# Kernel optimization log

Hardware: AMD Instinct MI355X
Metric: run time of the kernel (lower is better)

Reference implementation:

```python
import jax, jax.numpy as jnp
import numpy as np

B, H, W = 2, 512, 512
HID, NHKD, HEADS, KD, CD = 64, 128, 8, 16, 64
MAX_SHAPE = 512

def _conv(x, w, b=None, pad=0, groups=1):
    y = jax.lax.conv_general_dilated(x, w, (1, 1), [(pad, pad), (pad, pad)],
                                     dimension_numbers=('NCHW', 'OIHW', 'NCHW'),
                                     feature_group_count=groups)
    return y if b is None else y + b[None, :, None, None]

def _gelu(x):
    return jax.nn.gelu(x, approximate=False)  # torch nn.GELU default is exact erf

def _bn(x, s, t):
    # inference-mode BatchNorm folded to per-channel scale/shift
    return x * s[None, :, None, None] + t[None, :, None, None]

def _dyn_pos(xm, pe):
    # xm: (B, C, N); pe: (1, C, MAX_SHAPE); linear interp (align_corners=False) when N != MAX_SHAPE
    N = xm.shape[-1]
    if N != pe.shape[-1]:
        pe = jax.image.resize(pe, (1, pe.shape[1], N), method='linear')
    return xm + pe

def _sdpa(q, k, v):
    # q, k, v: (B, heads, L=key_dim, E=H); scale = 1/sqrt(E) as in F.scaled_dot_product_attention
    scale = 1.0 / np.sqrt(q.shape[-1])
    attn = jax.nn.softmax(jnp.einsum('bhie,bhje->bhij', q, k) * scale, axis=-1)
    return jnp.einsum('bhij,bhje->bhie', attn, v)

def setup_inputs():
    key = jax.random.key(0)
    ks = jax.random.split(key, 26)
    rn = lambda i, shp, sc=1.0: jax.random.normal(ks[i], shp, jnp.float32) * sc
    return {
        'x': rn(0, (B, HID, H, W)),
        'shortcut': rn(1, (B, CD, H, W)),
        'ln_w': jnp.ones((CD,), jnp.float32),
        'ln_b': jnp.zeros((CD,), jnp.float32),
        'dproj_dw_w': rn(2, (CD, 1, 3, 3), 0.2),
        'dproj_bn_s': 1.0 + rn(3, (CD,), 0.1),
        'dproj_bn_t': rn(4, (CD,), 0.1),
        'dproj_pw_w': rn(5, (2 * HID, CD, 1, 1), 0.125),
        'dproj_pw_b': rn(6, (2 * HID,), 0.05),
        'q_dw_w': rn(7, (NHKD, 1, 3, 3), 0.2),
        'q_bn_s': 1.0 + rn(8, (NHKD,), 0.1),
        'q_bn_t': rn(9, (NHKD,), 0.1),
        'k_dw_w': rn(10, (NHKD, 1, 3, 3), 0.2),
        'k_bn_s': 1.0 + rn(11, (NHKD,), 0.1),
        'k_bn_t': rn(12, (NHKD,), 0.1),
        'v_pw_w': rn(13, (NHKD, HID, 1, 1), 0.125),
        'v_bn_s': 1.0 + rn(14, (NHKD,), 0.1),
        'v_bn_t': rn(15, (NHKD,), 0.1),
        'proj_dw_w': rn(16, (HID + 2 * NHKD, 1, 3, 3), 0.2),
        'proj_dw_b': rn(17, (HID + 2 * NHKD,), 0.05),
        'proj_pw_w': rn(18, (HID, HID + 2 * NHKD, 1, 1), 0.06),
        'proj_pw_b': rn(19, (HID,), 0.05),
        'pe_rowq': rn(20, (1, NHKD, MAX_SHAPE), 0.02),
        'pe_rowk': rn(21, (1, NHKD, MAX_SHAPE), 0.02),
        'pe_colq': rn(22, (1, NHKD, MAX_SHAPE), 0.02),
        'pe_colk': rn(23, (1, NHKD, MAX_SHAPE), 0.02),
        'ape_row_w': jnp.ones((1, NHKD, 1, 1), jnp.float32),
        'ape_col_w': jnp.ones((1, NHKD, 1, 1), jnp.float32),
    }

def reference(x, shortcut, ln_w, ln_b, dproj_dw_w, dproj_bn_s, dproj_bn_t,
              dproj_pw_w, dproj_pw_b, q_dw_w, q_bn_s, q_bn_t, k_dw_w, k_bn_s,
              k_bn_t, v_pw_w, v_bn_s, v_bn_t, proj_dw_w, proj_dw_b, proj_pw_w,
              proj_pw_b, pe_rowq, pe_rowk, pe_colq, pe_colk, ape_row_w, ape_col_w):
    b, _, h, w = x.shape
    # LayerNorm2d: normalize over channel axis (biased variance, eps=1e-5)
    mu = shortcut.mean(axis=1, keepdims=True)
    var = shortcut.var(axis=1, keepdims=True)
    sn = (shortcut - mu) / jnp.sqrt(var + 1e-5) * ln_w[None, :, None, None] + ln_b[None, :, None, None]
    # d_proj: dw3x3 -> BN -> GELU -> pw1x1 -> GELU
    s = _gelu(_bn(_conv(sn, dproj_dw_w, pad=1, groups=CD), dproj_bn_s, dproj_bn_t))
    s = _gelu(_conv(s, dproj_pw_w, dproj_pw_b))
    k_in, v_in = jnp.split(s, 2, axis=1)  # each (B, HID, H, W)
    # q/k: grouped 3x3 conv (groups=HID, out=NHKD) -> BN -> GELU; v: 1x1 -> BN
    q = _gelu(_bn(_conv(x, q_dw_w, pad=1, groups=HID), q_bn_s, q_bn_t))
    k = _gelu(_bn(_conv(k_in, k_dw_w, pad=1, groups=HID), k_bn_s, k_bn_t))
    v = _bn(_conv(v_in, v_pw_w), v_bn_s, v_bn_t)
    # row attention: pool over W, seq dim = key_dim (16), head dim = H
    qr = _dyn_pos(q.mean(-1), pe_rowq).reshape(b, HEADS, KD, h)
    kr = _dyn_pos(k.mean(-1), pe_rowk).reshape(b, HEADS, KD, h)
    vr = v.mean(-1).reshape(b, HEADS, KD, h)
    attn_row = _sdpa(qr, kr, vr).reshape(b, NHKD, 1, h)
    # column attention: pool over H
    qc = _dyn_pos(q.mean(-2), pe_colq).reshape(b, HEADS, KD, w)
    kc = _dyn_pos(k.mean(-2), pe_colk).reshape(b, HEADS, KD, w)
    vc = v.mean(-2).reshape(b, HEADS, KD, w)
    attn_col = _sdpa(qc, kc, vc).reshape(b, NHKD, 1, w)
    # AxialPositionEncoding: both maps broadcast over spatial axis 2 (requires H == W)
    attn = v + ape_row_w * attn_row + ape_col_w * attn_col
    cat = jnp.concatenate([x, attn, v], axis=1)  # (B, 320, H, W)
    ctot = cat.shape[1]
    # channel shuffle: 'b (c g) h w -> b (g c) h w', g=5
    shuf = cat.reshape(b, ctot // 5, 5, h, w).transpose(0, 2, 1, 3, 4).reshape(b, ctot, h, w)
    p = _gelu(_conv(shuf, proj_dw_w, proj_dw_b, pad=1, groups=ctot))
    p = _conv(p, proj_pw_w, proj_pw_b)
    return _gelu(p)
```

## Files before the change

### kernel.cpp

```cpp
#include <hip/hip_runtime.h>
#include <math.h>

#define PLANE (512*512)

typedef short bf16x8 __attribute__((ext_vector_type(8)));
typedef float f32x4 __attribute__((ext_vector_type(4)));

__device__ __forceinline__ float gelu_f(float x) {
    float t2 = fmaf(x * x, 0.0713548162f, 1.5957691216f);
    float e = __expf(x * t2);
    float r = __builtin_amdgcn_rcpf(1.0f + e);
    return fmaf(-x, r, x);
}

__device__ __forceinline__ unsigned short f2bf(float f) {
    union { float f; unsigned u; } v; v.f = f;
    unsigned r = v.u + 0x7FFFu + ((v.u >> 16) & 1u);
    return (unsigned short)(r >> 16);
}

__device__ __forceinline__ float bf2f(unsigned short u) {
    union { unsigned u; float f; } x; x.u = ((unsigned)u) << 16; return x.f;
}

__device__ __forceinline__ float ldval(const float* p, int off) { return p[off]; }
__device__ __forceinline__ float ldval(const unsigned short* p, int off) { return bf2f(p[off]); }

__global__ __launch_bounds__(256) void k_lnstats(const float* __restrict__ sc,
                                                 float* __restrict__ Pb,
                                                 float* __restrict__ Qb) {
    int p = blockIdx.x * 256 + threadIdx.x;
    int b = p >> 18;
    int hw = p & (PLANE - 1);
    const float* src = sc + (size_t)b * 64 * PLANE + hw;
    float sum = 0.f, sq = 0.f;
    #pragma unroll 8
    for (int c = 0; c < 64; ++c) {
        float v = src[(size_t)c * PLANE];
        sum += v; sq += v * v;
    }
    float mu = sum * (1.0f / 64.0f);
    float var = sq * (1.0f / 64.0f) - mu * mu;
    float rstd = rsqrtf(var + 1e-5f);
    Pb[p] = rstd;
    Qb[p] = -mu * rstd;
}

__global__ __launch_bounds__(256) void k_dw64ln(const float* __restrict__ sc,
                                                const float* __restrict__ dww,
                                                const float* __restrict__ lnw,
                                                const float* __restrict__ lnb,
                                                const float* __restrict__ bns,
                                                const float* __restrict__ bnt,
                                                const float* __restrict__ Pb,
                                                const float* __restrict__ Qb,
                                                unsigned* __restrict__ t1b) {
    int p = blockIdx.x * 256 + threadIdx.x;
    int b = p >> 18;
    int hw = p & (PLANE - 1);
    int h = hw >> 9, w = hw & 511;
    int tapoff[9]; float Pt[9], Qt[9], vm[9];
    const float* Pp = Pb + (size_t)b * PLANE;
    const float* Qp = Qb + (size_t)b * PLANE;
    #pragma unroll
    for (int dh = -1; dh <= 1; ++dh)
        #pragma unroll
        for (int dw = -1; dw <= 1; ++dw) {
            int k = (dh + 1) * 3 + dw + 1;
            int hh = h + dh, ww = w + dw;
            bool ok = (hh >= 0 && hh < 512 && ww >= 0 && ww < 512);
            int hc = ok ? hh : h, wc = ok ? ww : w;
            int off = hc * 512 + wc;
            tapoff[k] = off;
            vm[k] = ok ? 1.f : 0.f;
            Pt[k] = Pp[off]; Qt[k] = Qp[off];
        }
    const float* scb = sc + (size_t)b * 64 * PLANE;
    unsigned* ob = t1b + (size_t)b * 32 * PLANE + hw;
    for (int c2 = 0; c2 < 32; ++c2) {
        float g[2];
        #pragma unroll
        for (int e = 0; e < 2; ++e) {
            int c = c2 * 2 + e;
            const float* wp = dww + c * 9;
            const float* cp = scb + (size_t)c * PLANE;
            float conv = 0.f, wsum = 0.f;
            #pragma unroll
            for (int k = 0; k < 9; ++k) {
                float wv = wp[k];
                float raw = cp[tapoff[k]];
                conv = fmaf(wv, fmaf(raw, Pt[k], Qt[k]) * vm[k], conv);
                wsum = fmaf(wv, vm[k], wsum);
            }
            float a = lnw[c] * conv + lnb[c] * wsum;
            g[e] = gelu_f(a * bns[c] + bnt[c]);
        }
        unsigned r;
        asm("v_cvt_pk_bf16_f32 %0,%1,%2" : "=v"(r) : "v"(g[0]), "v"(g[1]));
        ob[(size_t)c2 * PLANE] = r;
    }
}

__global__ __launch_bounds__(256) void k_wsetup2(const float* __restrict__ W1,
                                                 const float* __restrict__ W2,
                                                 unsigned short* __restrict__ w1b,
                                                 unsigned short* __restrict__ w2b) {
    int tid = blockIdx.x * 256 + threadIdx.x;
    if (tid < 8192) { w1b[tid] = f2bf(W1[tid]); w2b[tid] = f2bf(W2[tid]); }
}

__global__ __launch_bounds__(256, 4) void k_pw2(
    const unsigned* __restrict__ t1b,
    const unsigned short* __restrict__ w1b, const float* __restrict__ b1,
    const unsigned short* __restrict__ w2b,
    const float* __restrict__ vbs, const float* __restrict__ vbt,
    unsigned short* __restrict__ k_in, unsigned short* __restrict__ v)
{
    __shared__ unsigned short vin[64][88];
    __shared__ float epi[64 * 68];
    __shared__ float psl[128], ptl[128], pbl[128];
    int tid = threadIdx.x;
    if (tid < 128) { psl[tid] = vbs[tid]; ptl[tid] = vbt[tid]; pbl[tid] = b1[tid]; }
    int lane = tid & 63, wva = tid >> 6;
    int cl = lane & 15, kg = lane >> 4;
    int p0 = blockIdx.x * 64;
    int b = p0 >> 18;
    int hw0 = p0 & (PLANE - 1);
    int px = wva * 16 + cl;
    const unsigned* tp = t1b + (size_t)b * 32 * PLANE + hw0 + px;
    __syncthreads();

    unsigned bfr[2][4];
    #pragma unroll
    for (int ks = 0; ks < 2; ++ks)
        #pragma unroll
        for (int jp = 0; jp < 4; ++jp)
            bfr[ks][jp] = tp[(size_t)(ks * 16 + kg * 4 + jp) * PLANE];

    f32x4 acc[8];
    #pragma unroll
    for (int mt = 0; mt < 8; ++mt) acc[mt] = (f32x4){0.f, 0.f, 0.f, 0.f};
    #pragma unroll
    for (int ks = 0; ks < 2; ++ks) {
        union { unsigned u[4]; bf16x8 v; } bb;
        bb.u[0] = bfr[ks][0]; bb.u[1] = bfr[ks][1]; bb.u[2] = bfr[ks][2]; bb.u[3] = bfr[ks][3];
        #pragma unroll
        for (int mt = 0; mt < 8; ++mt) {
            bf16x8 af = *(const bf16x8*)(w1b + (size_t)(mt * 16 + cl) * 64 + ks * 32 + kg * 8);
            acc[mt] = __builtin_amdgcn_mfma_f32_16x16x32_bf16(af, bb.v, acc[mt], 0, 0, 0);
        }
    }

    #pragma unroll
    for (int mt = 4; mt < 8; ++mt) {
        float g[4];
        #pragma unroll
        for (int r = 0; r < 4; ++r)
            g[r] = gelu_f(acc[mt][r] + pbl[mt * 16 + kg * 4 + r]);
        unsigned r01, r23;
        asm("v_cvt_pk_bf16_f32 %0,%1,%2" : "=v"(r01) : "v"(g[0]), "v"(g[1]));
        asm("v_cvt_pk_bf16_f32 %0,%1,%2" : "=v"(r23) : "v"(g[2]), "v"(g[3]));
        int ch = (mt - 4) * 16 + kg * 4;
        *(unsigned*)&vin[px][ch]     = r01;
        *(unsigned*)&vin[px][ch + 2] = r23;
    }

    __syncthreads();
    #pragma unroll
    for (int mt = 0; mt < 4; ++mt)
        #pragma unroll
        for (int r = 0; r < 4; ++r) {
            int m = mt * 16 + kg * 4 + r;
            epi[m * 68 + px] = gelu_f(acc[mt][r] + pbl[m]);
        }
    __syncthreads();
    unsigned short* kb = k_in + (size_t)b * 64 * PLANE + hw0;
    #pragma unroll
    for (int k = 0; k < 4; ++k) {
        int m = wva * 16 + k * 4 + kg;
        float4 vv = *(const float4*)&epi[m * 68 + cl * 4];
        unsigned r01, r23;
        asm("v_cvt_pk_bf16_f32 %0,%1,%2" : "=v"(r01) : "v"(vv.x), "v"(vv.y));
        asm("v_cvt_pk_bf16_f32 %0,%1,%2" : "=v"(r23) : "v"(vv.z), "v"(vv.w));
        uint2 st; st.x = r01; st.y = r23;
        *(uint2*)&kb[(size_t)m * PLANE + cl * 4] = st;
    }

    f32x4 acc2[8];
    #pragma unroll
    for (int mt = 0; mt < 8; ++mt) acc2[mt] = (f32x4){0.f, 0.f, 0.f, 0.f};
    #pragma unroll
    for (int ks = 0; ks < 2; ++ks) {
        bf16x8 bb = *(const bf16x8*)&vin[px][ks * 32 + kg * 8];
        #pragma unroll
        for (int mt = 0; mt < 8; ++mt) {
            bf16x8 af = *(const bf16x8*)(w2b + (size_t)(mt * 16 + cl) * 64 + ks * 32 + kg * 8);
            acc2[mt] = __builtin_amdgcn_mfma_f32_16x16x32_bf16(af, bb, acc2[mt], 0, 0, 0);
        }
    }

    unsigned short* vb = v + (size_t)b * 128 * PLANE + hw0;
    #pragma unroll
    for (int pass = 0; pass < 2; ++pass) {
        __syncthreads();
        #pragma unroll
        for (int mt = pass * 4; mt < pass * 4 + 4; ++mt)
            #pragma unroll
            for (int r = 0; r < 4; ++r) {
                int m = mt * 16 + kg * 4 + r;
                epi[(m - pass * 64) * 68 + px] = acc2[mt][r] * psl[m] + ptl[m];
            }
        __syncthreads();
        #pragma unroll
        for (int k = 0; k < 4; ++k) {
            int ml = wva * 16 + k * 4 + kg;
            float4 vv = *(const float4*)&epi[ml * 68 + cl * 4];
            unsigned r01, r23;
            asm("v_cvt_pk_bf16_f32 %0,%1,%2" : "=v"(r01) : "v"(vv.x), "v"(vv.y));
            asm("v_cvt_pk_bf16_f32 %0,%1,%2" : "=v"(r23) : "v"(vv.z), "v"(vv.w));
            uint2 st; st.x = r01; st.y = r23;
            *(uint2*)&vb[(size_t)(pass * 64 + ml) * PLANE + cl * 4] = st;
        }
    }
}

template<typename T>
__global__ __launch_bounds__(512) void k_dwpool(const T* __restrict__ in,
                                                const float* __restrict__ wt,
                                                const float* __restrict__ bns,
                                                const float* __restrict__ bnt,
                                                float* __restrict__ rowsum,
                                                float* __restrict__ colpart) {
    __shared__ float lred[2][64][8];
    int tid = threadIdx.x;
    int blk = blockIdx.x;
    int hc = blk & 7;
    int g  = (blk >> 3) & 63;
    int b  = blk >> 9;
    int o0 = 2 * g, o1 = o0 + 1;
    const T* ip = in + ((size_t)b * 64 + g) * PLANE;
    float w0[9], w1[9];
    #pragma unroll
    for (int k = 0; k < 9; ++k) { w0[k] = wt[o0 * 9 + k]; w1[k] = wt[o1 * 9 + k]; }
    float s0 = bns[o0], t0 = bnt[o0], s1 = bns[o1], tt1 = bnt[o1];
    int w = tid;
    int wm = (w > 0)   ? w - 1 : w;  float vm0 = (w > 0)   ? 1.f : 0.f;
    int wp = (w < 511) ? w + 1 : w;  float vm2 = (w < 511) ? 1.f : 0.f;
    int h0 = hc * 64;
    int lane = tid & 63, wv = tid >> 6;
    float a0, a1, a2, r0, r1, r2, c0, c1, c2;
    if (h0 >= 1) {
        int o = (h0 - 1) * 512;
        a0 = ldval(ip, o + wm) * vm0; a1 = ldval(ip, o + w); a2 = ldval(ip, o + wp) * vm2;
    } else { a0 = a1 = a2 = 0.f; }
    {
        int o = h0 * 512;
        r0 = ldval(ip, o + wm) * vm0; r1 = ldval(ip, o + w); r2 = ldval(ip, o + wp) * vm2;
    }
    float ca0 = 0.f, ca1 = 0.f;
    for (int r = 0; r < 64; ++r) {
        int h = h0 + r;
        if (h + 1 <= 511) {
            int o = (h + 1) * 512;
            c0 = ldval(ip, o + wm) * vm0; c1 = ldval(ip, o + w); c2 = ldval(ip, o + wp) * vm2;
        } else { c0 = c1 = c2 = 0.f; }
        float x0 = w0[0]*a0 + w0[1]*a1 + w0[2]*a2 + w0[3]*r0 + w0[4]*r1 + w0[5]*r2
                 + w0[6]*c0 + w0[7]*c1 + w0[8]*c2;
        float x1 = w1[0]*a0 + w1[1]*a1 + w1[2]*a2 + w1[3]*r0 + w1[4]*r1 + w1[5]*r2
                 + w1[6]*c0 + w1[7]*c1 + w1[8]*c2;
        x0 = gelu_f(x0 * s0 + t0);
        x1 = gelu_f(x1 * s1 + tt1);
        ca0 += x0; ca1 += x1;
        #pragma unroll
        for (int off = 32; off > 0; off >>= 1) {
            x0 += __shfl_down(x0, off, 64);
            x1 += __shfl_down(x1, off, 64);
        }
        if (lane == 0) { lred[0][r][wv] = x0; lred[1][r][wv] = x1; }
        a0 = r0; a1 = r1; a2 = r2; r0 = c0; r1 = c1; r2 = c2;
    }
    colpart[((size_t)(b * 128 + o0) * 8 + hc) * 512 + w] = ca0;
    colpart[((size_t)(b * 128 + o1) * 8 + hc) * 512 + w] = ca1;
    __syncthreads();
    if (tid < 128) {
        int oo = tid >> 6, r = tid & 63;
        float s = 0.f;
        #pragma unroll
        for (int i = 0; i < 8; ++i) s += lred[oo][r][i];
        int och = oo ? o1 : o0;
        rowsum[((size_t)b * 128 + och) * 512 + h0 + r] = s;
    }
}

__global__ __launch_bounds__(512) void k_vpool(const unsigned short* __restrict__ v,
                                               float* __restrict__ rowsum,
                                               float* __restrict__ colpart) {
    __shared__ float lred[64][8];
    int tid = threadIdx.x;
    int blk = blockIdx.x;
    int hc = blk & 7;
    int c  = (blk >> 3) & 127;
    int b  = blk >> 10;
    int bc = b * 128 + c;
    const unsigned short* ip = v + (size_t)bc * PLANE;
    int h0 = hc * 64;
    int lane = tid & 63, wv = tid >> 6;
    float ca = 0.f;
    for (int r = 0; r < 64; ++r) {
        float a = bf2f(ip[(h0 + r) * 512 + tid]);
        ca += a;
        #pragma unroll
        for (int off = 32; off > 0; off >>= 1) a += __shfl_down(a, off, 64);
        if (lane == 0) lred[r][wv] = a;
    }
    colpart[((size_t)bc * 8 + hc) * 512 + tid] = ca;
    __syncthreads();
    if (tid < 64) {
        float s = 0.f;
        #pragma unroll
        for (int i = 0; i < 8; ++i) s += lred[tid][i];
        rowsum[(size_t)bc * 512 + h0 + tid] = s;
    }
}

__global__ __launch_bounds__(256) void k_colreduce(const float* __restrict__ part,
                                                   float* __restrict__ out, int n) {
    int idx = blockIdx.x * 256 + threadIdx.x;
    if (idx >= n) return;
    int bc = idx >> 9, w = idx & 511;
    const float* pp = part + ((size_t)bc * 8) * 512 + w;
    float s = 0.f;
    #pragma unroll
    for (int p = 0; p < 8; ++p) s += pp[p * 512];
    out[idx] = s;
}

__global__ __launch_bounds__(256) void k_attn(const float* __restrict__ qrow,
                                              const float* __restrict__ krow,
                                              const float* __restrict__ vrow,
                                              const float* __restrict__ qcol,
                                              const float* __restrict__ kcol,
                                              const float* __restrict__ vcol,
                                              const float* __restrict__ perq,
                                              const float* __restrict__ perk,
                                              const float* __restrict__ pecq,
                                              const float* __restrict__ peck,
                                              float* __restrict__ arow,
                                              float* __restrict__ acol) {
    __shared__ float Pj[16];
    __shared__ float Pe[16];
    int blk = blockIdx.x;
    int i    = blk & 15;
    int head = (blk >> 4) & 7;
    int axis = (blk >> 7) & 1;
    int b    = blk >> 8;
    const float* qs = axis ? qcol : qrow;
    const float* ks = axis ? kcol : krow;
    const float* vs = axis ? vcol : vrow;
    const float* peq = axis ? pecq : perq;
    const float* pek = axis ? peck : perk;
    float* out = axis ? acol : arow;
    int tid = threadIdx.x;
    int j = tid >> 4, l = tid & 15;
    int ci = head * 16 + i, cj = head * 16 + j;
    const float* qp = qs + ((size_t)b * 128 + ci) * 512;
    const float* kp = ks + ((size_t)b * 128 + cj) * 512;
    const float* qe = peq + ci * 512;
    const float* ke = pek + cj * 512;
    float s = 0.f;
    int n0 = l * 32;
    for (int n = n0; n < n0 + 32; ++n) {
        float qv = qp[n] * (1.f / 512.f) + qe[n];
        float kv = kp[n] * (1.f / 512.f) + ke[n];
        s = fmaf(qv, kv, s);
    }
    #pragma unroll
    for (int off = 8; off > 0; off >>= 1) s += __shfl_down(s, off, 16);
    if (l == 0) Pj[j] = s * 0.0441941738241592203f;
    __syncthreads();
    if (tid < 16) {
        float mx = -1e30f;
        #pragma unroll
        for (int jj = 0; jj < 16; ++jj) mx = fmaxf(mx, Pj[jj]);
        Pe[tid] = expf(Pj[tid] - mx);
    }
    __syncthreads();
    float sum = 0.f;
    #pragma unroll
    for (int jj = 0; jj < 16; ++jj) sum += Pe[jj];
    float inv = (1.f / 512.f) / sum;
    const float* vb = vs + ((size_t)b * 128 + head * 16) * 512;
    float* op = out + ((size_t)b * 128 + ci) * 512;
    #pragma unroll
    for (int rep = 0; rep < 2; ++rep) {
        int n = rep * 256 + tid;
        float acc = 0.f;
        #pragma unroll
        for (int jj = 0; jj < 16; ++jj)
            acc = fmaf(Pe[jj], vb[jj * 512 + n], acc);
        op[n] = acc * inv;
    }
}

__global__ __launch_bounds__(256) void k_wsetup(const float* __restrict__ pww,
                                                unsigned short* __restrict__ wsh) {
    int tid = blockIdx.x * 256 + threadIdx.x;
    if (tid >= 64 * 320) return;
    int m = tid / 320, src = tid % 320;
    int o = (src % 5) * 64 + src / 5;
    wsh[m * 320 + src] = f2bf(pww[m * 320 + o]);
}

__global__ __launch_bounds__(256) void k_awsetup(const float* __restrict__ pdw,
                                                 const float* __restrict__ aprw,
                                                 const float* __restrict__ apcw,
                                                 const float* __restrict__ arow,
                                                 const float* __restrict__ acol,
                                                 float* __restrict__ aw) {
    int idx = blockIdx.x * 256 + threadIdx.x;
    if (idx >= 2 * 128 * 512) return;
    int col = idx & 511;
    int c   = (idx >> 9) & 127;
    int b   = idx >> 16;
    int src = 64 + c;
    int o = (src % 5) * 64 + src / 5;
    const float* wd = pdw + o * 9;
    float ws0 = wd[0] + wd[3] + wd[6];
    float ws1 = wd[1] + wd[4] + wd[7];
    float ws2 = wd[2] + wd[5] + wd[8];
    const float* ar = arow + ((size_t)b * 128 + c) * 512;
    const float* ac = acol + ((size_t)b * 128 + c) * 512;
    float apr = aprw[c], apc = apcw[c];
    float sum = ws1 * (apr * ar[col] + apc * ac[col]);
    if (col > 0)   sum += ws0 * (apr * ar[col - 1] + apc * ac[col - 1]);
    if (col < 511) sum += ws2 * (apr * ar[col + 1] + apc * ac[col + 1]);
    aw[idx] = sum;
}

template<bool HE, bool WE>
__device__ __forceinline__ void conv2x2b(const unsigned short* __restrict__ p,
    const float* wlA, const float* wlP,
    const int* hrow, const float* rv, int ls, int rs, float cv0, float cv2,
    float outA[2], float outP[2])
{
    float a0,a1,a2, b0,b1,b2, c0,c1,c2;
    const unsigned short* q = p + hrow[0]*512;
    if (WE) { a0=bf2f(q[ls])*cv0; a1=bf2f(q[0]); a2=bf2f(q[rs])*cv2; } else { a0=bf2f(q[-1]); a1=bf2f(q[0]); a2=bf2f(q[1]); }
    q = p + hrow[1]*512;
    if (WE) { b0=bf2f(q[ls])*cv0; b1=bf2f(q[0]); b2=bf2f(q[rs])*cv2; } else { b0=bf2f(q[-1]); b1=bf2f(q[0]); b2=bf2f(q[1]); }
    q = p + hrow[2]*512;
    if (WE) { c0=bf2f(q[ls])*cv0; c1=bf2f(q[0]); c2=bf2f(q[rs])*cv2; } else { c0=bf2f(q[-1]); c1=bf2f(q[0]); c2=bf2f(q[1]); }
    #pragma unroll
    for (int hs = 0; hs < 2; ++hs) {
        float sA0 = wlA[0]*a0 + wlA[1]*a1 + wlA[2]*a2;
        float sA1 = wlA[3]*b0 + wlA[4]*b1 + wlA[5]*b2;
        float sA2 = wlA[6]*c0 + wlA[7]*c1 + wlA[8]*c2;
        float sP0 = wlP[0]*a0 + wlP[1]*a1 + wlP[2]*a2;
        float sP1 = wlP[3]*b0 + wlP[4]*b1 + wlP[5]*b2;
        float sP2 = wlP[6]*c0 + wlP[7]*c1 + wlP[8]*c2;
        if (HE) {
            outA[hs] = rv[hs]*sA0 + sA1 + rv[hs+2]*sA2 + wlA[9];
            outP[hs] = rv[hs]*sP0 + sP1 + rv[hs+2]*sP2 + wlP[9];
        } else {
            outA[hs] = sA0 + sA1 + sA2 + wlA[9];
            outP[hs] = sP0 + sP1 + sP2 + wlP[9];
        }
        if (hs < 1) {
            a0=b0; a1=b1; a2=b2; b0=c0; b1=c1; b2=c2;
            q = p + hrow[3]*512;
            if (WE) { c0=bf2f(q[ls])*cv0; c1=bf2f(q[0]); c2=bf2f(q[rs])*cv2; } else { c0=bf2f(q[-1]); c1=bf2f(q[0]); c2=bf2f(q[1]); }
        }
    }
}

template<bool HE, bool WE>
__device__ __forceinline__ void conv1x2(const float* __restrict__ p,
    const float* wl,
    const int* hrow, const float* rv, int ls, int rs, float cv0, float cv2,
    float out[2])
{
    float a0,a1,a2, b0,b1,b2, c0,c1,c2;
    const float* q = p + hrow[0]*512;
    if (WE) { a0=q[ls]*cv0; a1=q[0]; a2=q[rs]*cv2; } else { a0=q[-1]; a1=q[0]; a2=q[1]; }
    q = p + hrow[1]*512;
    if (WE) { b0=q[ls]*cv0; b1=q[0]; b2=q[rs]*cv2; } else { b0=q[-1]; b1=q[0]; b2=q[1]; }
    q = p + hrow[2]*512;
    if (WE) { c0=q[ls]*cv0; c1=q[0]; c2=q[rs]*cv2; } else { c0=q[-1]; c1=q[0]; c2=q[1]; }
    #pragma unroll
    for (int hs = 0; hs < 2; ++hs) {
        float s0 = wl[0]*a0 + wl[1]*a1 + wl[2]*a2;
        float s1 = wl[3]*b0 + wl[4]*b1 + wl[5]*b2;
        float s2 = wl[6]*c0 + wl[7]*c1 + wl[8]*c2;
        out[hs] = (HE ? (rv[hs]*s0 + s1 + rv[hs+2]*s2) : (s0 + s1 + s2)) + wl[9];
        if (hs < 1) {
            a0=b0; a1=b1; a2=b2; b0=c0; b1=c1; b2=c2;
            q = p + hrow[3]*512;
            if (WE) { c0=q[ls]*cv0; c1=q[0]; c2=q[rs]*cv2; } else { c0=q[-1]; c1=q[0]; c2=q[1]; }
        }
    }
}

template<bool HE, bool WE>
__device__ __forceinline__ void proj5_core(
    int h0, int wwbase, float* epi, const float* dwl,
    const float* __restrict__ xb, const unsigned short* __restrict__ vbp,
    const float* __restrict__ arb, const float* __restrict__ acb,
    const float* __restrict__ aprw, const float* __restrict__ apcw,
    const float* __restrict__ awb,
    const unsigned short* __restrict__ wsh, const float* __restrict__ pwb,
    float* __restrict__ outb)
{
    int tid = threadIdx.x;
    int lane = tid & 63, wva = tid >> 6;
    int cl = lane & 15, kg = lane >> 4;
    int ww = wwbase + wva * 16 + cl;

    int hrow[4]; float rv[4];
    #pragma unroll
    for (int i = 0; i < 4; ++i) {
        int r = h0 - 1 + i;
        float va = 1.f;
        if (HE) { if (r < 0) { r = 0; va = 0.f; } if (r > 511) { r = 511; va = 0.f; } }
        hrow[i] = r; rv[i] = va;
    }
    int ls = -1, rs = 1; float cv0 = 1.f, cv2 = 1.f;
    if (WE) {
        if (ww == 0)   { ls = 1;  cv0 = 0.f; }
        if (ww == 511) { rs = -1; cv2 = 0.f; }
    }

    f32x4 acc[2][4];
    #pragma unroll
    for (int hs = 0; hs < 2; ++hs)
        #pragma unroll
        for (int mt = 0; mt < 4; ++mt)
            acc[hs][mt] = (f32x4){0.f, 0.f, 0.f, 0.f};

    #pragma unroll
    for (int ks = 0; ks < 2; ++ks) {
        unsigned bp[2][4];
        #pragma unroll
        for (int jp = 0; jp < 4; ++jp) {
            float cj0[2], cj1[2];
            int ch = ks * 32 + kg * 8 + jp * 2;
            conv1x2<HE,WE>(xb + (size_t)ch * PLANE + ww, dwl + ch * 12,
                           hrow, rv, ls, rs, cv0, cv2, cj0);
            conv1x2<HE,WE>(xb + (size_t)(ch+1) * PLANE + ww, dwl + (ch+1) * 12,
                           hrow, rv, ls, rs, cv0, cv2, cj1);
            #pragma unroll
            for (int hs = 0; hs < 2; ++hs) {
                float g0 = gelu_f(cj0[hs]), g1 = gelu_f(cj1[hs]);
                unsigned r;
                asm("v_cvt_pk_bf16_f32 %0,%1,%2" : "=v"(r) : "v"(g0), "v"(g1));
                bp[hs][jp] = r;
            }
        }
        #pragma unroll
        for (int mt = 0; mt < 4; ++mt) {
            bf16x8 af = *(const bf16x8*)(wsh + (size_t)(mt * 16 + cl) * 320 + ks * 32 + kg * 8);
            #pragma unroll
            for (int hs = 0; hs < 2; ++hs) {
                union { unsigned u[4]; bf16x8 v; } bb;
                bb.u[0] = bp[hs][0]; bb.u[1] = bp[hs][1]; bb.u[2] = bp[hs][2]; bb.u[3] = bp[hs][3];
                acc[hs][mt] = __builtin_amdgcn_mfma_f32_16x16x32_bf16(af, bb.v, acc[hs][mt], 0, 0, 0);
            }
        }
    }

    #pragma unroll
    for (int vks = 0; vks < 4; ++vks) {
        unsigned bpA[2][4], bpP[2][4];
        #pragma unroll
        for (int jp = 0; jp < 4; ++jp) {
            float cA[2][2], cP[2][2];
            #pragma unroll
            for (int e = 0; e < 2; ++e) {
                int c = vks * 32 + kg * 8 + jp * 2 + e;
                const float* wlA = dwl + (64 + c) * 12;
                conv2x2b<HE,WE>(vbp + (size_t)c * PLANE + ww, wlA, dwl + (192 + c) * 12,
                                hrow, rv, ls, rs, cv0, cv2, cA[e], cP[e]);
                float awv = awb[(size_t)c * 512 + ww];
                #pragma unroll
                for (int hs = 0; hs < 2; ++hs) {
                    if (!HE) {
                        cA[e][hs] += awv;
                    } else {
                        if (rv[hs] + rv[hs + 2] == 2.f) {
                            cA[e][hs] += awv;
                        } else {
                            const float* arp = arb + (size_t)c * 512 + ww;
                            const float* acp = acb + (size_t)c * 512 + ww;
                            float apr = aprw[c], apc = apcw[c];
                            float aa0 = (apr * arp[ls] + apc * acp[ls]) * cv0;
                            float aa1 =  apr * arp[0]  + apc * acp[0];
                            float aa2 = (apr * arp[rs] + apc * acp[rs]) * cv2;
                            float wd0 = rv[hs]*wlA[0] + wlA[3] + rv[hs+2]*wlA[6];
                            float wd1 = rv[hs]*wlA[1] + wlA[4] + rv[hs+2]*wlA[7];
                            float wd2 = rv[hs]*wlA[2] + wlA[5] + rv[hs+2]*wlA[8];
                            cA[e][hs] += wd0*aa0 + wd1*aa1 + wd2*aa2;
                        }
                    }
                }
            }
            #pragma unroll
            for (int hs = 0; hs < 2; ++hs) {
                float gA0 = gelu_f(cA[0][hs]), gA1 = gelu_f(cA[1][hs]);
                float gP0 = gelu_f(cP[0][hs]), gP1 = gelu_f(cP[1][hs]);
                unsigned ra, rp;
                asm("v_cvt_pk_bf16_f32 %0,%1,%2" : "=v"(ra) : "v"(gA0), "v"(gA1));
                asm("v_cvt_pk_bf16_f32 %0,%1,%2" : "=v"(rp) : "v"(gP0), "v"(gP1));
                bpA[hs][jp] = ra; bpP[hs][jp] = rp;
            }
        }
        #pragma unroll
        for (int mt = 0; mt < 4; ++mt) {
            bf16x8 afA = *(const bf16x8*)(wsh + (size_t)(mt * 16 + cl) * 320 + (2 + vks) * 32 + kg * 8);
            #pragma unroll
            for (int hs = 0; hs < 2; ++hs) {
                union { unsigned u[4]; bf16x8 v; } bb;
                bb.u[0] = bpA[hs][0]; bb.u[1] = bpA[hs][1]; bb.u[2] = bpA[hs][2]; bb.u[3] = bpA[hs][3];
                acc[hs][mt] = __builtin_amdgcn_mfma_f32_16x16x32_bf16(afA, bb.v, acc[hs][mt], 0, 0, 0);
            }
            bf16x8 afP = *(const bf16x8*)(wsh + (size_t)(mt * 16 + cl) * 320 + (6 + vks) * 32 + kg * 8);
            #pragma unroll
            for (int hs = 0; hs < 2; ++hs) {
                union { unsigned u[4]; bf16x8 v; } bb;
                bb.u[0] = bpP[hs][0]; bb.u[1] = bpP[hs][1]; bb.u[2] = bpP[hs][2]; bb.u[3] = bpP[hs][3];
                acc[hs][mt] = __builtin_amdgcn_mfma_f32_16x16x32_bf16(afP, bb.v, acc[hs][mt], 0, 0, 0);
            }
        }
    }

    #pragma unroll
    for (int hs = 0; hs < 2; ++hs) {
        __syncthreads();
        #pragma unroll
        for (int mt = 0; mt < 4; ++mt)
            #pragma unroll
            for (int r = 0; r < 4; ++r) {
                int m = mt * 16 + kg * 4 + r;
                epi[m * 68 + wva * 16 + cl] = gelu_f(acc[hs][mt][r] + pwb[m]);
            }
        __syncthreads();
        #pragma unroll
        for (int k = 0; k < 4; ++k) {
            int m = wva * 16 + k * 4 + kg;
            float4 vv = *(const float4*)&epi[m * 68 + cl * 4];
            *(float4*)&outb[(size_t)m * PLANE + (size_t)(h0 + hs) * 512 + wwbase + cl * 4] = vv;
        }
    }
}

__global__ __launch_bounds__(256, 4) void k_proj5(
    const float* __restrict__ x, const unsigned short* __restrict__ v,
    const float* __restrict__ arow, const float* __restrict__ acol,
    const float* __restrict__ aprw, const float* __restrict__ apcw,
    const float* __restrict__ dww, const float* __restrict__ dwb,
    const unsigned short* __restrict__ wsh, const float* __restrict__ pwb,
    const float* __restrict__ aw, float* __restrict__ out)
{
    __shared__ float dwl[320 * 12];
    __shared__ float epi[64 * 68];
    int tid = threadIdx.x;
    for (int i = tid; i < 3200; i += 256) {
        int src = i / 10, k = i - src * 10;
        int o = (src % 5) * 64 + src / 5;
        dwl[src * 12 + k] = (k < 9) ? dww[o * 9 + k] : dwb[o];
    }
    __syncthreads();
    int flat = blockIdx.x;
    int nf = (flat & 7) * 512 + (flat >> 3);
    int bx = nf & 7;
    int s  = (nf >> 3) & 255;
    int b  = nf >> 11;
    int h0 = s * 2, wwbase = bx * 64;
    const float* xb  = x + (size_t)b * 64 * PLANE;
    const unsigned short* vbp = v + (size_t)b * 128 * PLANE;
    const float* arb = arow + (size_t)b * 128 * 512;
    const float* acb = acol + (size_t)b * 128 * 512;
    const float* awb = aw + (size_t)b * 128 * 512;
    float* outb = out + (size_t)b * 64 * PLANE;
    bool HEr = (s == 0) || (s == 255);
    bool WEr = (bx == 0) || (bx == 7);
    if (!HEr && !WEr)
        proj5_core<false,false>(h0, wwbase, epi, dwl, xb, vbp, arb, acb, aprw, apcw, awb, wsh, pwb, outb);
    else if (!HEr)
        proj5_core<false,true >(h0, wwbase, epi, dwl, xb, vbp, arb, acb, aprw, apcw, awb, wsh, pwb, outb);
    else
        proj5_core<true ,true >(h0, wwbase, epi, dwl, xb, vbp, arb, acb, aprw, apcw, awb, wsh, pwb, outb);
}

extern "C" void kernel_launch(void* const* d_in, const int* in_sizes, int n_in,
                              void* d_out, int out_size, void* d_ws, size_t ws_size,
                              hipStream_t stream) {
    const float* x    = (const float*)d_in[0];
    const float* sc   = (const float*)d_in[1];
    const float* lnw  = (const float*)d_in[2];
    const float* lnb  = (const float*)d_in[3];
    const float* ddw  = (const float*)d_in[4];
    const float* dbs  = (const float*)d_in[5];
    const float* dbt  = (const float*)d_in[6];
    const float* pw1  = (const float*)d_in[7];
    const float* pb1  = (const float*)d_in[8];
    const float* qdw  = (const float*)d_in[9];
    const float* qbs  = (const float*)d_in[10];
    const float* qbt  = (const float*)d_in[11];
    const float* kdw  = (const float*)d_in[12];
    const float* kbs  = (const float*)d_in[13];
    const float* kbt  = (const float*)d_in[14];
    const float* vpw  = (const float*)d_in[15];
    const float* vbs  = (const float*)d_in[16];
    const float* vbt  = (const float*)d_in[17];
    const float* pdw  = (const float*)d_in[18];
    const float* pdb  = (const float*)d_in[19];
    const float* ppw  = (const float*)d_in[20];
    const float* ppb  = (const float*)d_in[21];
    const float* perq = (const float*)d_in[22];
    const float* perk = (const float*)d_in[23];
    const float* pecq = (const float*)d_in[24];
    const float* peck = (const float*)d_in[25];
    const float* aprw = (const float*)d_in[26];
    const float* apcw = (const float*)d_in[27];

    unsigned short* kin_b = (unsigned short*)d_out;
    float* ws   = (float*)d_ws;
    float* bufB = ws;
    unsigned short* v_b = (unsigned short*)(ws + 33554432);
    float* sm   = ws + 100663296;
    float* qrow = sm;
    float* krow = sm + 131072;
    float* vrow = sm + 262144;
    float* qcol = sm + 393216;
    float* kcol = sm + 524288;
    float* vcol = sm + 655360;
    float* arow = sm + 786432;
    float* acol = sm + 917504;
    unsigned short* wsh = (unsigned short*)(ws + 101711872);
    float* aw   = ws + 101722112;
    unsigned short* w1b = (unsigned short*)(ws + 101853184);
    unsigned short* w2b = (unsigned short*)(ws + 101857280);
    float* Pb   = ws + 101861376;
    float* Qb   = ws + 102385664;
    unsigned* t1b = (unsigned*)bufB;
    float* qcp  = bufB;
    float* kcp  = bufB + 1048576;
    float* vcp  = bufB + 2097152;

    k_wsetup <<<80,   256, 0, stream>>>(ppw, wsh);
    k_wsetup2<<<32,   256, 0, stream>>>(pw1, vpw, w1b, w2b);
    k_lnstats<<<2048, 256, 0, stream>>>(sc, Pb, Qb);
    k_dw64ln <<<2048, 256, 0, stream>>>(sc, ddw, lnw, lnb, dbs, dbt, Pb, Qb, t1b);
    k_pw2    <<<8192, 256, 0, stream>>>(t1b, w1b, pb1, w2b, vbs, vbt, kin_b, v_b);
    k_dwpool<unsigned short><<<1024, 512, 0, stream>>>(kin_b, kdw, kbs, kbt, krow, kcp);
    k_vpool  <<<2048, 512, 0, stream>>>(v_b, vrow, vcp);
    k_dwpool<float><<<1024, 512, 0, stream>>>(x, qdw, qbs, qbt, qrow, qcp);
    k_colreduce<<<1536, 256, 0, stream>>>(qcp, qcol, 393216);
    k_attn   <<<512,  256, 0, stream>>>(qrow, krow, vrow, qcol, kcol, vcol,
                                        perq, perk, pecq, peck, arow, acol);
    k_awsetup<<<512,  256, 0, stream>>>(pdw, aprw, apcw, arow, acol, aw);
    k_proj5  <<<4096, 256, 0, stream>>>(x, v_b, arow, acol, aprw, apcw,
                                        pdw, pdb, wsh, ppb, aw, (float*)d_out);
}
```

Before: 856.3 us.

## Store v as channel-pair interleaved bf16 to widen loads in pool and proj

The v tensor is now written as pairs of adjacent channels packed into one 32-bit word per pixel instead of separate bf16 planes. k_vpool and the proj5 depthwise conv read one dword to get two channels, which halves the number of load instructions and lets vpool run with half the blocks. The pw2 epilogue is restructured to pack two channel rows into each output word and store with 16-byte writes. The cost is more register pressure in the conv helper, which now processes two channels at once.

```diff
diff --git a/kernel.cpp b/kernel.cpp
--- a/kernel.cpp
+++ b/kernel.cpp
@@ -114,7 +114,7 @@
     const unsigned short* __restrict__ w1b, const float* __restrict__ b1,
     const unsigned short* __restrict__ w2b,
     const float* __restrict__ vbs, const float* __restrict__ vbt,
-    unsigned short* __restrict__ k_in, unsigned short* __restrict__ v)
+    unsigned short* __restrict__ k_in, unsigned* __restrict__ vp)
 {
     __shared__ unsigned short vin[64][88];
     __shared__ float epi[64 * 68];
@@ -199,7 +199,7 @@
         }
     }
 
-    unsigned short* vb = v + (size_t)b * 128 * PLANE + hw0;
+    unsigned* vpb = vp + (size_t)b * 64 * PLANE + hw0;
     #pragma unroll
     for (int pass = 0; pass < 2; ++pass) {
         __syncthreads();
@@ -212,14 +212,19 @@
             }
         __syncthreads();
         #pragma unroll
-        for (int k = 0; k < 4; ++k) {
-            int ml = wva * 16 + k * 4 + kg;
-            float4 vv = *(const float4*)&epi[ml * 68 + cl * 4];
-            unsigned r01, r23;
-            asm("v_cvt_pk_bf16_f32 %0,%1,%2" : "=v"(r01) : "v"(vv.x), "v"(vv.y));
-            asm("v_cvt_pk_bf16_f32 %0,%1,%2" : "=v"(r23) : "v"(vv.z), "v"(vv.w));
-            uint2 st; st.x = r01; st.y = r23;
-            *(uint2*)&vb[(size_t)(pass * 64 + ml) * PLANE + cl * 4] = st;
+        for (int it = 0; it < 2; ++it) {
+            int idx = it * 256 + tid;
+            int pr = idx >> 4;
+            int seg = idx & 15;
+            const float* lo = &epi[(2 * pr) * 68 + seg * 4];
+            const float* hi = &epi[(2 * pr + 1) * 68 + seg * 4];
+            unsigned u0, u1, u2, u3;
+            asm("v_cvt_pk_bf16_f32 %0,%1,%2" : "=v"(u0) : "v"(lo[0]), "v"(hi[0]));
+            asm("v_cvt_pk_bf16_f32 %0,%1,%2" : "=v"(u1) : "v"(lo[1]), "v"(hi[1]));
+            asm("v_cvt_pk_bf16_f32 %0,%1,%2" : "=v"(u2) : "v"(lo[2]), "v"(hi[2]));
+            asm("v_cvt_pk_bf16_f32 %0,%1,%2" : "=v"(u3) : "v"(lo[3]), "v"(hi[3]));
+            uint4 st; st.x = u0; st.y = u1; st.z = u2; st.w = u3;
+            *(uint4*)&vpb[(size_t)(pass * 32 + pr) * PLANE + seg * 4] = st;
         }
     }
 }
@@ -292,34 +297,40 @@
     }
 }
 
-__global__ __launch_bounds__(512) void k_vpool(const unsigned short* __restrict__ v,
+__global__ __launch_bounds__(512) void k_vpool(const unsigned* __restrict__ vp,
                                                float* __restrict__ rowsum,
                                                float* __restrict__ colpart) {
-    __shared__ float lred[64][8];
+    __shared__ float lred[2][64][8];
     int tid = threadIdx.x;
     int blk = blockIdx.x;
     int hc = blk & 7;
-    int c  = (blk >> 3) & 127;
-    int b  = blk >> 10;
-    int bc = b * 128 + c;
-    const unsigned short* ip = v + (size_t)bc * PLANE;
+    int c2 = (blk >> 3) & 63;
+    int b  = blk >> 9;
+    const unsigned* ip = vp + ((size_t)b * 64 + c2) * PLANE;
     int h0 = hc * 64;
     int lane = tid & 63, wv = tid >> 6;
-    float ca = 0.f;
+    float ca0 = 0.f, ca1 = 0.f;
     for (int r = 0; r < 64; ++r) {
-        float a = bf2f(ip[(h0 + r) * 512 + tid]);
-        ca += a;
-        #pragma unroll
-        for (int off = 32; off > 0; off >>= 1) a += __shfl_down(a, off, 64);
-        if (lane == 0) lred[r][wv] = a;
-    }
-    colpart[((size_t)bc * 8 + hc) * 512 + tid] = ca;
+        unsigned u = ip[(h0 + r) * 512 + tid];
+        float a0 = bf2f((unsigned short)u);
+        float a1 = bf2f((unsigned short)(u >> 16));
+        ca0 += a0; ca1 += a1;
+        #pragma unroll
+        for (int off = 32; off > 0; off >>= 1) {
+            a0 += __shfl_down(a0, off, 64);
+            a1 += __shfl_down(a1, off, 64);
+        }
+        if (lane == 0) { lred[0][r][wv] = a0; lred[1][r][wv] = a1; }
+    }
+    colpart[((size_t)(b * 128 + 2 * c2)     * 8 + hc) * 512 + tid] = ca0;
+    colpart[((size_t)(b * 128 + 2 * c2 + 1) * 8 + hc) * 512 + tid] = ca1;
     __syncthreads();
-    if (tid < 64) {
+    if (tid < 128) {
+        int oo = tid >> 6, r = tid & 63;
         float s = 0.f;
         #pragma unroll
-        for (int i = 0; i < 8; ++i) s += lred[tid][i];
-        rowsum[(size_t)bc * 512 + h0 + tid] = s;
+        for (int i = 0; i < 8; ++i) s += lred[oo][r][i];
+        rowsum[((size_t)b * 128 + 2 * c2 + oo) * 512 + h0 + r] = s;
     }
 }
 
@@ -438,39 +449,59 @@
 }
 
 template<bool HE, bool WE>
-__device__ __forceinline__ void conv2x2b(const unsigned short* __restrict__ p,
-    const float* wlA, const float* wlP,
+__device__ __forceinline__ void conv4x2b(const unsigned* __restrict__ p,
+    const float* wA0, const float* wP0, const float* wA1, const float* wP1,
     const int* hrow, const float* rv, int ls, int rs, float cv0, float cv2,
-    float outA[2], float outP[2])
+    float oA[2][2], float oP[2][2])
 {
-    float a0,a1,a2, b0,b1,b2, c0,c1,c2;
-    const unsigned short* q = p + hrow[0]*512;
-    if (WE) { a0=bf2f(q[ls])*cv0; a1=bf2f(q[0]); a2=bf2f(q[rs])*cv2; } else { a0=bf2f(q[-1]); a1=bf2f(q[0]); a2=bf2f(q[1]); }
-    q = p + hrow[1]*512;
-    if (WE) { b0=bf2f(q[ls])*cv0; b1=bf2f(q[0]); b2=bf2f(q[rs])*cv2; } else { b0=bf2f(q[-1]); b1=bf2f(q[0]); b2=bf2f(q[1]); }
-    q = p + hrow[2]*512;
-    if (WE) { c0=bf2f(q[ls])*cv0; c1=bf2f(q[0]); c2=bf2f(q[rs])*cv2; } else { c0=bf2f(q[-1]); c1=bf2f(q[0]); c2=bf2f(q[1]); }
+    float aL0,aC0,aR0, aL1,aC1,aR1;
+    float bL0,bC0,bR0, bL1,bC1,bR1;
+    float cL0,cC0,cR0, cL1,cC1,cR1;
+    const unsigned* q;
+#define LDROW(L0,C0,R0,L1,C1,R1) do { \
+        unsigned uL = WE ? q[ls] : q[-1]; \
+        unsigned uC = q[0]; \
+        unsigned uR = WE ? q[rs] : q[1]; \
+        L0 = bf2f((unsigned short)uL); L1 = bf2f((unsigned short)(uL >> 16)); \
+        C0 = bf2f((unsigned short)uC); C1 = bf2f((unsigned short)(uC >> 16)); \
+        R0 = bf2f((unsigned short)uR); R1 = bf2f((unsigned short)(uR >> 16)); \
+        if (WE) { L0 *= cv0; L1 *= cv0; R0 *= cv2; R1 *= cv2; } \
+    } while (0)
+    q = p + hrow[0] * 512; LDROW(aL0,aC0,aR0,aL1,aC1,aR1);
+    q = p + hrow[1] * 512; LDROW(bL0,bC0,bR0,bL1,bC1,bR1);
+    q = p + hrow[2] * 512; LDROW(cL0,cC0,cR0,cL1,cC1,cR1);
     #pragma unroll
     for (int hs = 0; hs < 2; ++hs) {
-        float sA0 = wlA[0]*a0 + wlA[1]*a1 + wlA[2]*a2;
-        float sA1 = wlA[3]*b0 + wlA[4]*b1 + wlA[5]*b2;
-        float sA2 = wlA[6]*c0 + wlA[7]*c1 + wlA[8]*c2;
-        float sP0 = wlP[0]*a0 + wlP[1]*a1 + wlP[2]*a2;
-        float sP1 = wlP[3]*b0 + wlP[4]*b1 + wlP[5]*b2;
-        float sP2 = wlP[6]*c0 + wlP[7]*c1 + wlP[8]*c2;
+        float tA0 = wA0[0]*aL0 + wA0[1]*aC0 + wA0[2]*aR0;
+        float mA0 = wA0[3]*bL0 + wA0[4]*bC0 + wA0[5]*bR0;
+        float dA0 = wA0[6]*cL0 + wA0[7]*cC0 + wA0[8]*cR0;
+        float tP0 = wP0[0]*aL0 + wP0[1]*aC0 + wP0[2]*aR0;
+        float mP0 = wP0[3]*bL0 + wP0[4]*bC0 + wP0[5]*bR0;
+        float dP0 = wP0[6]*cL0 + wP0[7]*cC0 + wP0[8]*cR0;
+        float tA1 = wA1[0]*aL1 + wA1[1]*aC1 + wA1[2]*aR1;
+        float mA1 = wA1[3]*bL1 + wA1[4]*bC1 + wA1[5]*bR1;
+        float dA1 = wA1[6]*cL1 + wA1[7]*cC1 + wA1[8]*cR1;
+        float tP1 = wP1[0]*aL1 + wP1[1]*aC1 + wP1[2]*aR1;
+        float mP1 = wP1[3]*bL1 + wP1[4]*bC1 + wP1[5]*bR1;
+        float dP1 = wP1[6]*cL1 + wP1[7]*cC1 + wP1[8]*cR1;
         if (HE) {
-            outA[hs] = rv[hs]*sA0 + sA1 + rv[hs+2]*sA2 + wlA[9];
-            outP[hs] = rv[hs]*sP0 + sP1 + rv[hs+2]*sP2 + wlP[9];
+            oA[0][hs] = rv[hs]*tA0 + mA0 + rv[hs+2]*dA0 + wA0[9];
+            oP[0][hs] = rv[hs]*tP0 + mP0 + rv[hs+2]*dP0 + wP0[9];
+            oA[1][hs] = rv[hs]*tA1 + mA1 + rv[hs+2]*dA1 + wA1[9];
+            oP[1][hs] = rv[hs]*tP1 + mP1 + rv[hs+2]*dP1 + wP1[9];
         } else {
-            outA[hs] = sA0 + sA1 + sA2 + wlA[9];
-            outP[hs] = sP0 + sP1 + sP2 + wlP[9];
+            oA[0][hs] = tA0 + mA0 + dA0 + wA0[9];
+            oP[0][hs] = tP0 + mP0 + dP0 + wP0[9];
+            oA[1][hs] = tA1 + mA1 + dA1 + wA1[9];
+            oP[1][hs] = tP1 + mP1 + dP1 + wP1[9];
         }
         if (hs < 1) {
-            a0=b0; a1=b1; a2=b2; b0=c0; b1=c1; b2=c2;
-            q = p + hrow[3]*512;
-            if (WE) { c0=bf2f(q[ls])*cv0; c1=bf2f(q[0]); c2=bf2f(q[rs])*cv2; } else { c0=bf2f(q[-1]); c1=bf2f(q[0]); c2=bf2f(q[1]); }
-        }
-    }
+            aL0=bL0; aC0=bC0; aR0=bR0; aL1=bL1; aC1=bC1; aR1=bR1;
+            bL0=cL0; bC0=cC0; bR0=cR0; bL1=cL1; bC1=cC1; bR1=cR1;
+            q = p + hrow[3] * 512; LDROW(cL0,cC0,cR0,cL1,cC1,cR1);
+        }
+    }
+#undef LDROW
 }
 
 template<bool HE, bool WE>
@@ -503,7 +534,7 @@
 template<bool HE, bool WE>
 __device__ __forceinline__ void proj5_core(
     int h0, int wwbase, float* epi, const float* dwl,
-    const float* __restrict__ xb, const unsigned short* __restrict__ vbp,
+    const float* __restrict__ xb, const unsigned* __restrict__ vbp,
     const float* __restrict__ arb, const float* __restrict__ acb,
     const float* __restrict__ aprw, const float* __restrict__ apcw,
     const float* __restrict__ awb,
@@ -572,14 +603,16 @@
         unsigned bpA[2][4], bpP[2][4];
         #pragma unroll
         for (int jp = 0; jp < 4; ++jp) {
+            int c = vks * 32 + kg * 8 + jp * 2;
+            int pr = c >> 1;
             float cA[2][2], cP[2][2];
+            conv4x2b<HE,WE>(vbp + (size_t)pr * PLANE + ww,
+                            dwl + (64 + c) * 12,  dwl + (192 + c) * 12,
+                            dwl + (64 + c + 1) * 12, dwl + (192 + c + 1) * 12,
+                            hrow, rv, ls, rs, cv0, cv2, cA, cP);
             #pragma unroll
             for (int e = 0; e < 2; ++e) {
-                int c = vks * 32 + kg * 8 + jp * 2 + e;
-                const float* wlA = dwl + (64 + c) * 12;
-                conv2x2b<HE,WE>(vbp + (size_t)c * PLANE + ww, wlA, dwl + (192 + c) * 12,
-                                hrow, rv, ls, rs, cv0, cv2, cA[e], cP[e]);
-                float awv = awb[(size_t)c * 512 + ww];
+                float awv = awb[(size_t)(c + e) * 512 + ww];
                 #pragma unroll
                 for (int hs = 0; hs < 2; ++hs) {
                     if (!HE) {
@@ -588,9 +621,10 @@
                         if (rv[hs] + rv[hs + 2] == 2.f) {
                             cA[e][hs] += awv;
                         } else {
-                            const float* arp = arb + (size_t)c * 512 + ww;
-                            const float* acp = acb + (size_t)c * 512 + ww;
-                            float apr = aprw[c], apc = apcw[c];
+                            const float* wlA = dwl + (64 + c + e) * 12;
+                            const float* arp = arb + (size_t)(c + e) * 512 + ww;
+                            const float* acp = acb + (size_t)(c + e) * 512 + ww;
+                            float apr = aprw[c + e], apc = apcw[c + e];
                             float aa0 = (apr * arp[ls] + apc * acp[ls]) * cv0;
                             float aa1 =  apr * arp[0]  + apc * acp[0];
                             float aa2 = (apr * arp[rs] + apc * acp[rs]) * cv2;
@@ -652,7 +686,7 @@
 }
 
 __global__ __launch_bounds__(256, 4) void k_proj5(
-    const float* __restrict__ x, const unsigned short* __restrict__ v,
+    const float* __restrict__ x, const unsigned* __restrict__ vp,
     const float* __restrict__ arow, const float* __restrict__ acol,
     const float* __restrict__ aprw, const float* __restrict__ apcw,
     const float* __restrict__ dww, const float* __restrict__ dwb,
@@ -675,7 +709,7 @@
     int b  = nf >> 11;
     int h0 = s * 2, wwbase = bx * 64;
     const float* xb  = x + (size_t)b * 64 * PLANE;
-    const unsigned short* vbp = v + (size_t)b * 128 * PLANE;
+    const unsigned* vbp = vp + (size_t)b * 64 * PLANE;
     const float* arb = arow + (size_t)b * 128 * 512;
     const float* acb = acol + (size_t)b * 128 * 512;
     const float* awb = aw + (size_t)b * 128 * 512;
@@ -725,7 +759,7 @@
     unsigned short* kin_b = (unsigned short*)d_out;
     float* ws   = (float*)d_ws;
     float* bufB = ws;
-    unsigned short* v_b = (unsigned short*)(ws + 33554432);
+    unsigned* vp_b = (unsigned*)(ws + 33554432);
     float* sm   = ws + 100663296;
     float* qrow = sm;
     float* krow = sm + 131072;
@@ -750,14 +784,14 @@
     k_wsetup2<<<32,   256, 0, stream>>>(pw1, vpw, w1b, w2b);
     k_lnstats<<<2048, 256, 0, stream>>>(sc, Pb, Qb);
     k_dw64ln <<<2048, 256, 0, stream>>>(sc, ddw, lnw, lnb, dbs, dbt, Pb, Qb, t1b);
-    k_pw2    <<<8192, 256, 0, stream>>>(t1b, w1b, pb1, w2b, vbs, vbt, kin_b, v_b);
+    k_pw2    <<<8192, 256, 0, stream>>>(t1b, w1b, pb1, w2b, vbs, vbt, kin_b, vp_b);
     k_dwpool<unsigned short><<<1024, 512, 0, stream>>>(kin_b, kdw, kbs, kbt, krow, kcp);
-    k_vpool  <<<2048, 512, 0, stream>>>(v_b, vrow, vcp);
+    k_vpool  <<<1024, 512, 0, stream>>>(vp_b, vrow, vcp);
     k_dwpool<float><<<1024, 512, 0, stream>>>(x, qdw, qbs, qbt, qrow, qcp);
     k_colreduce<<<1536, 256, 0, stream>>>(qcp, qcol, 393216);
     k_attn   <<<512,  256, 0, stream>>>(qrow, krow, vrow, qcol, kcol, vcol,
                                         perq, perk, pecq, peck, arow, acol);
     k_awsetup<<<512,  256, 0, stream>>>(pdw, aprw, apcw, arow, acol, aw);
-    k_proj5  <<<4096, 256, 0, stream>>>(x, v_b, arow, acol, aprw, apcw,
+    k_proj5  <<<4096, 256, 0, stream>>>(x, vp_b, arow, acol, aprw, apcw,
                                         pdw, pdb, wsh, ppb, aw, (float*)d_out);
 }
```

New measurement: 869.6 us. Within noise of the previous version (+1.6%).
